# Performance work log

Hardware: AMD Instinct MI355X
Metric: run time of the kernel (lower is better)

Reference implementation:

```python
import jax, jax.numpy as jnp
import numpy as np
import math

EMBED_DIM = 1024
NUM_HEADS = 16
HEAD_DIM = EMBED_DIM // NUM_HEADS  # 64
BLOCK = 64
SPARSITY = 0.05
BATCH = 2
SEQ = 2048


def _block_pattern(seq_len, block_size, sparsity_ratio, is_causal):
    """Faithful replication of _create_hilbert_aware_block_pattern (use_hilbert_pattern=True)."""
    nb = seq_len // block_size
    total = nb * nb
    keep = int(total * (1.0 - sparsity_ratio))
    idx = [(i, i) for i in range(nb)]
    band = max(1, int(math.sqrt(keep - nb) / 2))
    for i in range(nb):
        for o in range(1, band + 1):
            if i + o < nb:
                idx.append((i, i + o))
                if not is_causal:
                    idx.append((i + o, i))
            if (not is_causal) and i - o >= 0:
                idx.append((i, i - o))
    for skip in (2, 4, 8, 16):
        if len(idx) >= keep:
            break
        for i in range(0, nb - skip, skip):
            if len(idx) < keep:
                idx.append((i, i + skip))
                if (not is_causal) and len(idx) < keep:
                    idx.append((i + skip, i))
    uniq = sorted(set(idx))  # set-dedup as in original; sorted for determinism (no truncation occurs at these sizes)
    if is_causal:
        uniq = [(r, c) for r, c in uniq if r >= c]
    uniq = uniq[:keep]
    rows = np.array([r for r, c in uniq], dtype=np.int32)
    cols = np.array([c for r, c in uniq], dtype=np.int32)
    return rows, cols


ROWS, COLS = _block_pattern(SEQ, BLOCK, SPARSITY, is_causal=False)  # P = 752 blocks


def setup_inputs() -> dict:
    rng = jax.random.key(0)
    ks = jax.random.split(rng, 7)
    wscale = EMBED_DIM ** -0.5  # keep pre-softmax logits in a sane range
    return {
        "query": jax.random.normal(ks[0], (BATCH, SEQ, EMBED_DIM), jnp.float32),
        "key": jax.random.normal(ks[1], (BATCH, SEQ, EMBED_DIM), jnp.float32),
        "value": jax.random.normal(ks[2], (BATCH, SEQ, EMBED_DIM), jnp.float32),
        "Wq": jax.random.normal(ks[3], (EMBED_DIM, EMBED_DIM), jnp.float32) * wscale,
        "Wk": jax.random.normal(ks[4], (EMBED_DIM, EMBED_DIM), jnp.float32) * wscale,
        "Wv": jax.random.normal(ks[5], (EMBED_DIM, EMBED_DIM), jnp.float32) * wscale,
        "Wo": jax.random.normal(ks[6], (EMBED_DIM, EMBED_DIM), jnp.float32) * wscale,
    }


def reference(query, key, value, Wq, Wk, Wv, Wo):
    B, S, E = query.shape
    nb = S // BLOCK
    scale = HEAD_DIM ** -0.5

    def proj_blocks(x, W):
        # [B,S,E] -> [B,H,nb,block,hd]
        h = (x @ W.T).reshape(B, S, NUM_HEADS, HEAD_DIM).transpose(0, 2, 1, 3)
        return h.reshape(B, NUM_HEADS, nb, BLOCK, HEAD_DIM)

    qb = proj_blocks(query, Wq)
    kb = proj_blocks(key, Wk)
    vb = proj_blocks(value, Wv)

    rows = jnp.asarray(ROWS)
    cols = jnp.asarray(COLS)
    qg = qb[:, :, rows]  # [B,H,P,block,hd]
    kg = kb[:, :, cols]
    vg = vb[:, :, cols]

    # Per-block softmax (NOT online softmax across column blocks) exactly as the torch loop
    scores = jnp.einsum('bhpqd,bhpkd->bhpqk', qg, kg) * scale  # [B,H,P,block,block]
    attn = jax.nn.softmax(scores, axis=-1)
    ob = jnp.einsum('bhpqk,bhpkd->bhpqd', attn, vg)  # [B,H,P,block,hd]

    # Accumulate (sum) contributions into each query row block, as the torch += loop does
    acc = jax.ops.segment_sum(ob.transpose(2, 0, 1, 3, 4), rows, num_segments=nb)  # [nb,B,H,block,hd]
    out = acc.transpose(1, 2, 0, 3, 4).reshape(B, NUM_HEADS, S, HEAD_DIM)
    out = out.transpose(0, 2, 1, 3).reshape(B, S, E)
    return out @ Wo.T
```

## Files before the change

### kernel.cpp

```cpp
#include <hip/hip_runtime.h>
#include <hip/hip_bf16.h>

typedef __attribute__((ext_vector_type(4))) float f32x4;
typedef __attribute__((ext_vector_type(8))) short bfx8;

#define K_DIM 1024
#define N_DIM 1024

__device__ __forceinline__ ushort f2bf(float f) {
    uint u = __float_as_uint(f);
    u += 0x7fffu + ((u >> 16) & 1u);
    return (ushort)(u >> 16);
}

__device__ __forceinline__ uint pk2bf(float lo, float hi) {
    __hip_bfloat162 h = __float22bfloat162_rn(float2{lo, hi});
    uint r;
    __builtin_memcpy(&r, &h, 4);
    return r;
}

__device__ __forceinline__ void gll16(const ushort* g, ushort* l) {
    __builtin_amdgcn_global_load_lds(
        (const __attribute__((address_space(1))) uint*)g,
        (__attribute__((address_space(3))) uint*)l,
        16, 0, 0);
}

template<int CTRL>
__device__ __forceinline__ float dpp_add(float x) {
    int yi = __builtin_amdgcn_update_dpp(0, __float_as_int(x), CTRL, 0xf, 0xf, true);
    return x + __int_as_float(yi);
}

__device__ __forceinline__ int frag_off(int lane, int kk) {
    return (lane & 15)*128 + (((kk<<2) + (lane >> 4)) ^ (lane & 7))*16;
}

__global__ __launch_bounds__(256) void cvt_w(
    const float* __restrict__ wq, const float* __restrict__ wk,
    const float* __restrict__ wv, const float* __restrict__ wo,
    ushort* __restrict__ ws)
{
    const int W4 = 1 << 18;
    const int total = 4*W4;
    ushort4* dst4 = reinterpret_cast<ushort4*>(ws);
    for (int u = blockIdx.x*blockDim.x + threadIdx.x; u < total; u += gridDim.x*blockDim.x) {
        int op = u >> 18;
        int local = u & (W4-1);
        const float* src = op==0 ? wq : (op==1 ? wk : (op==2 ? wv : wo));
        float4 f = reinterpret_cast<const float4*>(src)[local];
        ushort4 o;
        o.x = f2bf(f.x); o.y = f2bf(f.y); o.z = f2bf(f.z); o.w = f2bf(f.w);
        dst4[u] = o;
    }
}

template<int MODE>
__device__ __forceinline__ void gemm_body(
    const float* __restrict__ Af, const ushort* __restrict__ Ab,
    const ushort* __restrict__ Bw,
    ushort* __restrict__ C, float* __restrict__ Cf,
    int blk, ushort* As, ushort* Bs)
{
    const int tid  = threadIdx.x;
    const int lane = tid & 63;
    const int wave = tid >> 6;
    const int tn = blk & 7;
    const int tm = blk >> 3;
    const int wr = wave >> 1, wc = wave & 1;

    int goff[4];
    #pragma unroll
    for (int t = 0; t < 4; ++t) {
        int u = wave*256 + t*64 + lane;
        int row = u >> 3;
        int col = (u & 7) ^ (row & 7);
        goff[t] = row * K_DIM + col * 8;
    }
    const int fo0 = frag_off(lane, 0), fo1 = frag_off(lane, 1);
    const ushort* Bbase  = Bw + (size_t)tn * 128 * K_DIM;
    const float*  Afbase = (MODE < 2) ? Af + (size_t)tm * 128 * K_DIM : nullptr;
    const ushort* Abbase = (MODE == 2) ? Ab + (size_t)tm * 128 * K_DIM : nullptr;

    f32x4 acc[4][4];
    #pragma unroll
    for (int a = 0; a < 4; ++a)
        #pragma unroll
        for (int b2 = 0; b2 < 4; ++b2)
            acc[a][b2] = (f32x4){0.f, 0.f, 0.f, 0.f};

    for (int k0 = 0; k0 < K_DIM; k0 += 64) {
        __syncthreads();
        #pragma unroll
        for (int t = 0; t < 4; ++t)
            gll16(Bbase + k0 + goff[t], Bs + (wave*256 + t*64)*8);
        if constexpr (MODE == 2) {
            #pragma unroll
            for (int t = 0; t < 4; ++t)
                gll16(Abbase + k0 + goff[t], As + (wave*256 + t*64)*8);
        } else {
            #pragma unroll
            for (int t = 0; t < 4; ++t) {
                int u = tid + t*256;
                int row = u >> 3, col = u & 7;
                const float* s = Afbase + (size_t)row*K_DIM + k0 + col*8;
                float4 f0 = *reinterpret_cast<const float4*>(s);
                float4 f1 = *reinterpret_cast<const float4*>(s + 4);
                uint4 packed;
                packed.x = pk2bf(f0.x, f0.y);
                packed.y = pk2bf(f0.z, f0.w);
                packed.z = pk2bf(f1.x, f1.y);
                packed.w = pk2bf(f1.z, f1.w);
                *reinterpret_cast<uint4*>(&As[row*64 + (col ^ (row & 7))*8]) = packed;
            }
        }
        __syncthreads();
        #pragma unroll
        for (int kk = 0; kk < 2; ++kk) {
            const int fo = kk ? fo1 : fo0;
            const char* ap = (const char*)As + wr*8192 + fo;
            const char* bp = (const char*)Bs + wc*8192 + fo;
            bfx8 af[4], bfr[4];
            #pragma unroll
            for (int mi = 0; mi < 4; ++mi)
                af[mi] = *reinterpret_cast<const bfx8*>(ap + mi*2048);
            #pragma unroll
            for (int ni = 0; ni < 4; ++ni)
                bfr[ni] = *reinterpret_cast<const bfx8*>(bp + ni*2048);
            #pragma unroll
            for (int mi = 0; mi < 4; ++mi)
                #pragma unroll
                for (int ni = 0; ni < 4; ++ni)
                    acc[mi][ni] = __builtin_amdgcn_mfma_f32_16x16x32_bf16(af[mi], bfr[ni], acc[mi][ni], 0, 0, 0);
        }
    }
    #pragma unroll
    for (int mi = 0; mi < 4; ++mi)
      #pragma unroll
      for (int ni = 0; ni < 4; ++ni)
        #pragma unroll
        for (int i = 0; i < 4; ++i) {
            int gr = tm*128 + wr*64 + mi*16 + (lane >> 4)*4 + i;
            int gc = tn*128 + wc*64 + ni*16 + (lane & 15);
            if constexpr (MODE == 0) {
                int b = gr >> 11, s = gr & 2047, h = gc >> 6, d = gc & 63;
                C[(((size_t)(b*16 + h))*2048 + s)*64 + d] = f2bf(acc[mi][ni][i]);
            } else if constexpr (MODE == 1) {
                int b = gr >> 11, s = gr & 2047, h = gc >> 6, d = gc & 63;
                C[(((size_t)(b*16 + h))*64 + d)*2048 + s] = f2bf(acc[mi][ni][i]);
            } else {
                Cf[(size_t)gr*N_DIM + gc] = acc[mi][ni][i];
            }
        }
}

__global__ __launch_bounds__(256) void proj_kernel(
    const float* __restrict__ q, const float* __restrict__ k, const float* __restrict__ v,
    const ushort* __restrict__ wqb, const ushort* __restrict__ wkb, const ushort* __restrict__ wvb,
    ushort* __restrict__ Qp, ushort* __restrict__ Kp, ushort* __restrict__ Vt)
{
    __shared__ ushort As[128*64];
    __shared__ ushort Bs[128*64];
    int wgid = (blockIdx.x & 7) * 96 + (blockIdx.x >> 3);
    int op = wgid >> 8;
    int t  = wgid & 255;
    if (op == 0)      gemm_body<0>(q, nullptr, wqb, Qp, nullptr, t, As, Bs);
    else if (op == 1) gemm_body<0>(k, nullptr, wkb, Kp, nullptr, t, As, Bs);
    else              gemm_body<1>(v, nullptr, wvb, Vt, nullptr, t, As, Bs);
}

__global__ __launch_bounds__(256) void outproj_kernel(
    const ushort* __restrict__ AO, const ushort* __restrict__ wob, float* __restrict__ out)
{
    __shared__ ushort As[128*64];
    __shared__ ushort Bs[128*64];
    int wgid = (blockIdx.x & 7) * 32 + (blockIdx.x >> 3);
    gemm_body<2>(nullptr, AO, wob, nullptr, out, wgid, As, Bs);
}

__global__ __launch_bounds__(512) void attn_kernel(
    const ushort* __restrict__ Qp, const ushort* __restrict__ Kp,
    const ushort* __restrict__ Vt, ushort* __restrict__ AO)
{
    const int wgid = (blockIdx.x & 7) * 64 + (blockIdx.x >> 3);
    const int g = wgid & 15;
    const int h = (wgid >> 4) & 15;
    const int b = wgid >> 8;
    const int r0 = g << 1;
    const int tid  = threadIdx.x;
    const int lane = tid & 63;
    const int wave = tid >> 6;
    const int rw = r0 + (wave >> 2);

    __shared__ ushort Ks[2][4096];
    __shared__ ushort Vs[2][4096];
    __shared__ ushort QPs[8192];

    const ushort* Qb = Qp + (size_t)(b*16 + h) * 2048 * 64;
    const ushort* Kb = Kp + (size_t)(b*16 + h) * 2048 * 64;
    const ushort* Vb = Vt + (size_t)(b*16 + h) * 64 * 2048;

    const int krow = tid >> 3;
    const int kcol = (tid & 7) ^ (krow & 7);
    const int koff = krow*64   + kcol*8;
    const int voff = krow*2048 + kcol*8;
    const int fo0 = frag_off(lane, 0), fo1 = frag_off(lane, 1);

    int clo = r0 - 15; if (clo < 0) clo = 0;
    int chi = r0 + 16; if (chi > 31) chi = 31;

    #pragma unroll
    for (int t = 0; t < 2; ++t) {
        int u = wave*128 + t*64 + lane;
        int row = u >> 3;
        int col = (u & 7) ^ (row & 7);
        gll16(Qb + (size_t)(r0*64 + row)*64 + col*8, QPs + (wave*128 + t*64)*8);
    }
    gll16(Kb + (size_t)clo*4096 + koff, &Ks[0][wave*64*8]);
    gll16(Vb + (size_t)clo*64   + voff, &Vs[0][wave*64*8]);
    __syncthreads();

    const char* qp_base = (const char*)QPs + wave*2048;
    bfx8 qf[2];
    qf[0] = *reinterpret_cast<const bfx8*>(qp_base + fo0);
    qf[1] = *reinterpret_cast<const bfx8*>(qp_base + fo1);

    f32x4 acc_o[4];
    #pragma unroll
    for (int n = 0; n < 4; ++n) acc_o[n] = (f32x4){0.f,0.f,0.f,0.f};

    const float SC = 0.125f * 1.44269504f;
    int cur = 0;
    for (int c = clo; c <= chi; ++c) {
        if (c < chi) {
            gll16(Kb + (size_t)(c+1)*4096 + koff, &Ks[cur^1][wave*64*8]);
            gll16(Vb + (size_t)(c+1)*64   + voff, &Vs[cur^1][wave*64*8]);
        }

        if (c >= rw - 15 && c <= rw + 15) {
            const char* kcur = (const char*)&Ks[cur][0];
            f32x4 sc[4];
            #pragma unroll
            for (int n = 0; n < 4; ++n) sc[n] = (f32x4){0.f,0.f,0.f,0.f};
            #pragma unroll
            for (int kk = 0; kk < 2; ++kk) {
                const char* kp = kcur + (kk ? fo1 : fo0);
                bfx8 kf[4];
                #pragma unroll
                for (int n = 0; n < 4; ++n)
                    kf[n] = *reinterpret_cast<const bfx8*>(kp + n*2048);
                __builtin_amdgcn_s_setprio(1);
                #pragma unroll
                for (int n = 0; n < 4; ++n)
                    sc[n] = __builtin_amdgcn_mfma_f32_16x16x32_bf16(qf[kk], kf[n], sc[n], 0,0,0);
                __builtin_amdgcn_s_setprio(0);
            }

            float pn[4][4]; float inv[4];
            #pragma unroll
            for (int i = 0; i < 4; ++i) {
                float ssum = 0.f;
                #pragma unroll
                for (int n = 0; n < 4; ++n) { float e = exp2f(sc[n][i]*SC); pn[n][i] = e; ssum += e; }
                ssum = dpp_add<0xB1>(ssum);
                ssum = dpp_add<0x4E>(ssum);
                ssum = dpp_add<0x124>(ssum);
                ssum = dpp_add<0x128>(ssum);
                inv[i] = __builtin_amdgcn_rcpf(ssum);
            }
            #pragma unroll
            for (int n = 0; n < 4; ++n) {
                int colv = n*16 + (lane & 15);
                #pragma unroll
                for (int ip = 0; ip < 2; ++ip) {
                    uint w = pk2bf(pn[n][2*ip]*inv[2*ip], pn[n][2*ip+1]*inv[2*ip+1]);
                    int row0 = wave*16 + (lane >> 4)*4 + 2*ip;
                    QPs[row0*64     + ((colv >> 3) ^ ( row0    & 7))*8 + (colv & 7)] = (ushort)w;
                    QPs[(row0+1)*64 + ((colv >> 3) ^ ((row0+1) & 7))*8 + (colv & 7)] = (ushort)(w >> 16);
                }
            }

            const char* vcur = (const char*)&Vs[cur][0];
            #pragma unroll
            for (int kk = 0; kk < 2; ++kk) {
                const int fo = kk ? fo1 : fo0;
                bfx8 pf = *reinterpret_cast<const bfx8*>(qp_base + fo);
                const char* vp = vcur + fo;
                bfx8 vf[4];
                #pragma unroll
                for (int n = 0; n < 4; ++n)
                    vf[n] = *reinterpret_cast<const bfx8*>(vp + n*2048);
                __builtin_amdgcn_s_setprio(1);
                #pragma unroll
                for (int n = 0; n < 4; ++n)
                    acc_o[n] = __builtin_amdgcn_mfma_f32_16x16x32_bf16(pf, vf[n], acc_o[n], 0,0,0);
                __builtin_amdgcn_s_setprio(0);
            }
        }

        __syncthreads();
        cur ^= 1;
    }

    #pragma unroll
    for (int n = 0; n < 4; ++n)
        #pragma unroll
        for (int i = 0; i < 4; ++i) {
            int qrow = r0*64 + wave*16 + (lane >> 4)*4 + i;
            int e    = h*64 + n*16 + (lane & 15);
            AO[((size_t)b*2048 + qrow)*1024 + e] = f2bf(acc_o[n][i]);
        }
}

extern "C" void kernel_launch(void* const* d_in, const int* in_sizes, int n_in,
                              void* d_out, int out_size, void* d_ws, size_t ws_size,
                              hipStream_t stream)
{
    (void)in_sizes; (void)n_in; (void)out_size; (void)ws_size;
    const float* q  = (const float*)d_in[0];
    const float* k  = (const float*)d_in[1];
    const float* v  = (const float*)d_in[2];
    const float* wq = (const float*)d_in[3];
    const float* wk = (const float*)d_in[4];
    const float* wv = (const float*)d_in[5];
    const float* wo = (const float*)d_in[6];

    ushort* ws = (ushort*)d_ws;
    const size_t IN_E = 4096ull * 1024ull;
    const size_t W_E  = 1024ull * 1024ull;
    ushort* wqb = ws;
    ushort* wkb = wqb + W_E;
    ushort* wvb = wkb + W_E;
    ushort* wob = wvb + W_E;
    ushort* Qp  = wob + W_E;
    ushort* Kp  = Qp + IN_E;
    ushort* Vt  = Kp + IN_E;
    ushort* AO  = Vt + IN_E;

    cvt_w<<<1024, 256, 0, stream>>>(wq, wk, wv, wo, ws);
    proj_kernel<<<768, 256, 0, stream>>>(q, k, v, wqb, wkb, wvb, Qp, Kp, Vt);
    attn_kernel<<<512, 512, 0, stream>>>(Qp, Kp, Vt, AO);
    outproj_kernel<<<256, 256, 0, stream>>>(AO, wob, (float*)d_out);
}
```

Baseline: 248.9 us.

## Halve attention waves, give each wave two query sub-tiles, fold softmax scale into Q

The attention kernel now runs 256 threads per workgroup instead of 512, and each wave handles 32 query rows as two 16-row sub-tiles. Each K/V fragment read from LDS therefore feeds twice as many MFMAs, cutting LDS traffic per unit of work. Separately, the softmax scale and log2(e) factor are multiplied into Q in the projection epilogue, which removes a multiply per score element. The costs are higher register pressure, fewer waves per workgroup to hide latency, and Q rounded to bf16 after scaling.

```diff
diff --git a/kernel.cpp b/kernel.cpp
--- a/kernel.cpp
+++ b/kernel.cpp
@@ -61,7 +61,7 @@
     const float* __restrict__ Af, const ushort* __restrict__ Ab,
     const ushort* __restrict__ Bw,
     ushort* __restrict__ C, float* __restrict__ Cf,
-    int blk, ushort* As, ushort* Bs)
+    int blk, ushort* As, ushort* Bs, float ascale)
 {
     const int tid  = threadIdx.x;
     const int lane = tid & 63;
@@ -145,7 +145,7 @@
             int gc = tn*128 + wc*64 + ni*16 + (lane & 15);
             if constexpr (MODE == 0) {
                 int b = gr >> 11, s = gr & 2047, h = gc >> 6, d = gc & 63;
-                C[(((size_t)(b*16 + h))*2048 + s)*64 + d] = f2bf(acc[mi][ni][i]);
+                C[(((size_t)(b*16 + h))*2048 + s)*64 + d] = f2bf(acc[mi][ni][i]*ascale);
             } else if constexpr (MODE == 1) {
                 int b = gr >> 11, s = gr & 2047, h = gc >> 6, d = gc & 63;
                 C[(((size_t)(b*16 + h))*64 + d)*2048 + s] = f2bf(acc[mi][ni][i]);
@@ -162,12 +162,13 @@
 {
     __shared__ ushort As[128*64];
     __shared__ ushort Bs[128*64];
+    const float SC = 0.125f * 1.44269504f;
     int wgid = (blockIdx.x & 7) * 96 + (blockIdx.x >> 3);
     int op = wgid >> 8;
     int t  = wgid & 255;
-    if (op == 0)      gemm_body<0>(q, nullptr, wqb, Qp, nullptr, t, As, Bs);
-    else if (op == 1) gemm_body<0>(k, nullptr, wkb, Kp, nullptr, t, As, Bs);
-    else              gemm_body<1>(v, nullptr, wvb, Vt, nullptr, t, As, Bs);
+    if (op == 0)      gemm_body<0>(q, nullptr, wqb, Qp, nullptr, t, As, Bs, SC);
+    else if (op == 1) gemm_body<0>(k, nullptr, wkb, Kp, nullptr, t, As, Bs, 1.0f);
+    else              gemm_body<1>(v, nullptr, wvb, Vt, nullptr, t, As, Bs, 1.0f);
 }
 
 __global__ __launch_bounds__(256) void outproj_kernel(
@@ -176,10 +177,10 @@
     __shared__ ushort As[128*64];
     __shared__ ushort Bs[128*64];
     int wgid = (blockIdx.x & 7) * 32 + (blockIdx.x >> 3);
-    gemm_body<2>(nullptr, AO, wob, nullptr, out, wgid, As, Bs);
-}
-
-__global__ __launch_bounds__(512) void attn_kernel(
+    gemm_body<2>(nullptr, AO, wob, nullptr, out, wgid, As, Bs, 1.0f);
+}
+
+__global__ __launch_bounds__(256) void attn_kernel(
     const ushort* __restrict__ Qp, const ushort* __restrict__ Kp,
     const ushort* __restrict__ Vt, ushort* __restrict__ AO)
 {
@@ -191,7 +192,7 @@
     const int tid  = threadIdx.x;
     const int lane = tid & 63;
     const int wave = tid >> 6;
-    const int rw = r0 + (wave >> 2);
+    const int rw = r0 + (wave >> 1);
 
     __shared__ ushort Ks[2][4096];
     __shared__ ushort Vs[2][4096];
@@ -201,48 +202,65 @@
     const ushort* Kb = Kp + (size_t)(b*16 + h) * 2048 * 64;
     const ushort* Vb = Vt + (size_t)(b*16 + h) * 64 * 2048;
 
-    const int krow = tid >> 3;
-    const int kcol = (tid & 7) ^ (krow & 7);
-    const int koff = krow*64   + kcol*8;
-    const int voff = krow*2048 + kcol*8;
+    int koff[2], voff[2];
+    #pragma unroll
+    for (int t = 0; t < 2; ++t) {
+        int u = tid + t*256;
+        int row = u >> 3;
+        int col = (u & 7) ^ (row & 7);
+        koff[t] = row*64   + col*8;
+        voff[t] = row*2048 + col*8;
+    }
     const int fo0 = frag_off(lane, 0), fo1 = frag_off(lane, 1);
 
     int clo = r0 - 15; if (clo < 0) clo = 0;
     int chi = r0 + 16; if (chi > 31) chi = 31;
 
     #pragma unroll
-    for (int t = 0; t < 2; ++t) {
-        int u = wave*128 + t*64 + lane;
+    for (int t = 0; t < 4; ++t) {
+        int u = tid + t*256;
         int row = u >> 3;
         int col = (u & 7) ^ (row & 7);
-        gll16(Qb + (size_t)(r0*64 + row)*64 + col*8, QPs + (wave*128 + t*64)*8);
-    }
-    gll16(Kb + (size_t)clo*4096 + koff, &Ks[0][wave*64*8]);
-    gll16(Vb + (size_t)clo*64   + voff, &Vs[0][wave*64*8]);
+        gll16(Qb + (size_t)(r0*64 + row)*64 + col*8, QPs + ((wave + 4*t)*64)*8);
+    }
+    #pragma unroll
+    for (int t = 0; t < 2; ++t) {
+        gll16(Kb + (size_t)clo*4096 + koff[t], &Ks[0][((wave + 4*t)*64)*8]);
+        gll16(Vb + (size_t)clo*64   + voff[t], &Vs[0][((wave + 4*t)*64)*8]);
+    }
     __syncthreads();
 
-    const char* qp_base = (const char*)QPs + wave*2048;
-    bfx8 qf[2];
-    qf[0] = *reinterpret_cast<const bfx8*>(qp_base + fo0);
-    qf[1] = *reinterpret_cast<const bfx8*>(qp_base + fo1);
-
-    f32x4 acc_o[4];
-    #pragma unroll
-    for (int n = 0; n < 4; ++n) acc_o[n] = (f32x4){0.f,0.f,0.f,0.f};
-
-    const float SC = 0.125f * 1.44269504f;
+    const char* qp_base = (const char*)QPs + wave*4096;
+    bfx8 qf[2][2];
+    #pragma unroll
+    for (int sub = 0; sub < 2; ++sub) {
+        qf[sub][0] = *reinterpret_cast<const bfx8*>(qp_base + sub*2048 + fo0);
+        qf[sub][1] = *reinterpret_cast<const bfx8*>(qp_base + sub*2048 + fo1);
+    }
+
+    f32x4 acc_o[2][4];
+    #pragma unroll
+    for (int sub = 0; sub < 2; ++sub)
+        #pragma unroll
+        for (int n = 0; n < 4; ++n) acc_o[sub][n] = (f32x4){0.f,0.f,0.f,0.f};
+
     int cur = 0;
     for (int c = clo; c <= chi; ++c) {
         if (c < chi) {
-            gll16(Kb + (size_t)(c+1)*4096 + koff, &Ks[cur^1][wave*64*8]);
-            gll16(Vb + (size_t)(c+1)*64   + voff, &Vs[cur^1][wave*64*8]);
+            #pragma unroll
+            for (int t = 0; t < 2; ++t) {
+                gll16(Kb + (size_t)(c+1)*4096 + koff[t], &Ks[cur^1][((wave + 4*t)*64)*8]);
+                gll16(Vb + (size_t)(c+1)*64   + voff[t], &Vs[cur^1][((wave + 4*t)*64)*8]);
+            }
         }
 
         if (c >= rw - 15 && c <= rw + 15) {
             const char* kcur = (const char*)&Ks[cur][0];
-            f32x4 sc[4];
-            #pragma unroll
-            for (int n = 0; n < 4; ++n) sc[n] = (f32x4){0.f,0.f,0.f,0.f};
+            f32x4 sc[2][4];
+            #pragma unroll
+            for (int sub = 0; sub < 2; ++sub)
+                #pragma unroll
+                for (int n = 0; n < 4; ++n) sc[sub][n] = (f32x4){0.f,0.f,0.f,0.f};
             #pragma unroll
             for (int kk = 0; kk < 2; ++kk) {
                 const char* kp = kcur + (kk ? fo1 : fo0);
@@ -252,49 +270,59 @@
                     kf[n] = *reinterpret_cast<const bfx8*>(kp + n*2048);
                 __builtin_amdgcn_s_setprio(1);
                 #pragma unroll
-                for (int n = 0; n < 4; ++n)
-                    sc[n] = __builtin_amdgcn_mfma_f32_16x16x32_bf16(qf[kk], kf[n], sc[n], 0,0,0);
+                for (int sub = 0; sub < 2; ++sub)
+                    #pragma unroll
+                    for (int n = 0; n < 4; ++n)
+                        sc[sub][n] = __builtin_amdgcn_mfma_f32_16x16x32_bf16(qf[sub][kk], kf[n], sc[sub][n], 0,0,0);
                 __builtin_amdgcn_s_setprio(0);
             }
 
-            float pn[4][4]; float inv[4];
-            #pragma unroll
-            for (int i = 0; i < 4; ++i) {
-                float ssum = 0.f;
-                #pragma unroll
-                for (int n = 0; n < 4; ++n) { float e = exp2f(sc[n][i]*SC); pn[n][i] = e; ssum += e; }
-                ssum = dpp_add<0xB1>(ssum);
-                ssum = dpp_add<0x4E>(ssum);
-                ssum = dpp_add<0x124>(ssum);
-                ssum = dpp_add<0x128>(ssum);
-                inv[i] = __builtin_amdgcn_rcpf(ssum);
-            }
-            #pragma unroll
-            for (int n = 0; n < 4; ++n) {
-                int colv = n*16 + (lane & 15);
-                #pragma unroll
-                for (int ip = 0; ip < 2; ++ip) {
-                    uint w = pk2bf(pn[n][2*ip]*inv[2*ip], pn[n][2*ip+1]*inv[2*ip+1]);
-                    int row0 = wave*16 + (lane >> 4)*4 + 2*ip;
-                    QPs[row0*64     + ((colv >> 3) ^ ( row0    & 7))*8 + (colv & 7)] = (ushort)w;
-                    QPs[(row0+1)*64 + ((colv >> 3) ^ ((row0+1) & 7))*8 + (colv & 7)] = (ushort)(w >> 16);
+            float pn[2][4][4]; float inv[2][4];
+            #pragma unroll
+            for (int sub = 0; sub < 2; ++sub)
+                #pragma unroll
+                for (int i = 0; i < 4; ++i) {
+                    float ssum = 0.f;
+                    #pragma unroll
+                    for (int n = 0; n < 4; ++n) { float e = exp2f(sc[sub][n][i]); pn[sub][n][i] = e; ssum += e; }
+                    ssum = dpp_add<0xB1>(ssum);
+                    ssum = dpp_add<0x4E>(ssum);
+                    ssum = dpp_add<0x124>(ssum);
+                    ssum = dpp_add<0x128>(ssum);
+                    inv[sub][i] = __builtin_amdgcn_rcpf(ssum);
                 }
-            }
+            #pragma unroll
+            for (int sub = 0; sub < 2; ++sub)
+                #pragma unroll
+                for (int n = 0; n < 4; ++n) {
+                    int colv = n*16 + (lane & 15);
+                    #pragma unroll
+                    for (int ip = 0; ip < 2; ++ip) {
+                        uint w = pk2bf(pn[sub][n][2*ip]*inv[sub][2*ip], pn[sub][n][2*ip+1]*inv[sub][2*ip+1]);
+                        int row0 = wave*32 + sub*16 + (lane >> 4)*4 + 2*ip;
+                        QPs[row0*64     + ((colv >> 3) ^ ( row0    & 7))*8 + (colv & 7)] = (ushort)w;
+                        QPs[(row0+1)*64 + ((colv >> 3) ^ ((row0+1) & 7))*8 + (colv & 7)] = (ushort)(w >> 16);
+                    }
+                }
 
             const char* vcur = (const char*)&Vs[cur][0];
             #pragma unroll
             for (int kk = 0; kk < 2; ++kk) {
                 const int fo = kk ? fo1 : fo0;
-                bfx8 pf = *reinterpret_cast<const bfx8*>(qp_base + fo);
                 const char* vp = vcur + fo;
                 bfx8 vf[4];
                 #pragma unroll
                 for (int n = 0; n < 4; ++n)
                     vf[n] = *reinterpret_cast<const bfx8*>(vp + n*2048);
+                bfx8 pf[2];
+                pf[0] = *reinterpret_cast<const bfx8*>(qp_base + fo);
+                pf[1] = *reinterpret_cast<const bfx8*>(qp_base + 2048 + fo);
                 __builtin_amdgcn_s_setprio(1);
                 #pragma unroll
-                for (int n = 0; n < 4; ++n)
-                    acc_o[n] = __builtin_amdgcn_mfma_f32_16x16x32_bf16(pf, vf[n], acc_o[n], 0,0,0);
+                for (int sub = 0; sub < 2; ++sub)
+                    #pragma unroll
+                    for (int n = 0; n < 4; ++n)
+                        acc_o[sub][n] = __builtin_amdgcn_mfma_f32_16x16x32_bf16(pf[sub], vf[n], acc_o[sub][n], 0,0,0);
                 __builtin_amdgcn_s_setprio(0);
             }
         }
@@ -304,13 +332,15 @@
     }
 
     #pragma unroll
-    for (int n = 0; n < 4; ++n)
-        #pragma unroll
-        for (int i = 0; i < 4; ++i) {
-            int qrow = r0*64 + wave*16 + (lane >> 4)*4 + i;
-            int e    = h*64 + n*16 + (lane & 15);
-            AO[((size_t)b*2048 + qrow)*1024 + e] = f2bf(acc_o[n][i]);
-        }
+    for (int sub = 0; sub < 2; ++sub)
+        #pragma unroll
+        for (int n = 0; n < 4; ++n)
+            #pragma unroll
+            for (int i = 0; i < 4; ++i) {
+                int qrow = r0*64 + wave*32 + sub*16 + (lane >> 4)*4 + i;
+                int e    = h*64 + n*16 + (lane & 15);
+                AO[((size_t)b*2048 + qrow)*1024 + e] = f2bf(acc_o[sub][n][i]);
+            }
 }
 
 extern "C" void kernel_launch(void* const* d_in, const int* in_sizes, int n_in,
@@ -340,6 +370,6 @@
 
     cvt_w<<<1024, 256, 0, stream>>>(wq, wk, wv, wo, ws);
     proj_kernel<<<768, 256, 0, stream>>>(q, k, v, wqb, wkb, wvb, Qp, Kp, Vt);
-    attn_kernel<<<512, 512, 0, stream>>>(Qp, Kp, Vt, AO);
+    attn_kernel<<<512, 256, 0, stream>>>(Qp, Kp, Vt, AO);
     outproj_kernel<<<256, 256, 0, stream>>>(AO, wob, (float*)d_out);
 }
```

Measured after the change: 255.7 us. 2.8% more time.
